# Kernel optimization log

Measured on AMD Instinct MI355X. Metric: run time of the kernel, lower is better.

Reference implementation:

```python
import jax, jax.numpy as jnp
import numpy as np

B, M, HID, NH = 2, 2048, 1024, 16
D = HID // NH  # 64


def setup_inputs() -> dict:
    key = jax.random.key(0)
    ks = jax.random.split(key, 6)
    s = 0.02  # weight init scale
    return {
        "h": jax.random.normal(ks[0], (B, M, HID), dtype=jnp.float32),
        "key_pe": jax.random.normal(ks[1], (1, D, M), dtype=jnp.float32) * s,
        "Wq": jax.random.normal(ks[2], (HID, HID), dtype=jnp.float32) * s,
        "Wk": jax.random.normal(ks[3], (HID, HID), dtype=jnp.float32) * s,
        "Wv": jax.random.normal(ks[4], (HID, HID), dtype=jnp.float32) * s,
        "Wo": jax.random.normal(ks[5], (HID, HID), dtype=jnp.float32) * s,
    }


def reference(h, key_pe, Wq, Wk, Wv, Wo):
    # Faithful to the source: in SelfAttention.forward the gathered-span scores
    # are overwritten by dense Q K^T, and the softmaxed `attn` is discarded;
    # the returned value is (Q K^T) V (no scaling, no softmax). key_pe only
    # feeds the dead softmax branch, so it does not affect the output.
    b, m, hd = h.shape
    nh, d = NH, hd // NH

    def heads(x):  # (B, M, HID) -> (B, NH, M, D)
        return x.reshape(b, m, nh, d).transpose(0, 2, 1, 3)

    q = heads(h @ Wq.T)
    k = heads(h @ Wk.T)
    v = heads(h @ Wv.T)

    attn_cont = jnp.einsum("bhqd,bhkd->bhqk", q, k)  # (B, NH, M, M)
    out = jnp.einsum("bhqk,bhkd->bhqd", attn_cont, v)  # (B, NH, M, D)
    out = out.transpose(0, 2, 1, 3).reshape(b, m, hd)  # (B, M, HID)
    return out @ Wo.T
```

## Files before the change

### kernel.cpp

```cpp
#include <hip/hip_runtime.h>
#include <hip/hip_bf16.h>


typedef unsigned short u16;
typedef unsigned int u32;
typedef __attribute__((ext_vector_type(8))) short bf16x8;
typedef __attribute__((ext_vector_type(4))) float f32x4;

__device__ __forceinline__ void async_copy16(void* lds, const void* g) {
  __builtin_amdgcn_global_load_lds((const __attribute__((address_space(1))) void*)g,
                                   (__attribute__((address_space(3))) void*)lds,
                                   16, 0, 0);
}

__device__ __forceinline__ u16 f2bf(float f) {
  union { __hip_bfloat16 h; u16 u; } c;
  c.h = __float2bfloat16(f);
  return c.u;
}
__device__ __forceinline__ float bflo(u32 w) {
  union { u32 u; float f; } c; c.u = w << 16; return c.f;
}
__device__ __forceinline__ float bfhi(u32 w) {
  union { u32 u; float f; } c; c.u = w & 0xFFFF0000u; return c.f;
}
__device__ __forceinline__ ushort4 cvt4(float4 v) {
  ushort4 o; o.x = f2bf(v.x); o.y = f2bf(v.y); o.z = f2bf(v.z); o.w = f2bf(v.w);
  return o;
}

template <int N> __device__ __forceinline__ void vw() {
  if constexpr (N == 8)      asm volatile("s_waitcnt vmcnt(8)" ::: "memory");
  else if constexpr (N == 4) asm volatile("s_waitcnt vmcnt(4)" ::: "memory");
  else if constexpr (N == 2) asm volatile("s_waitcnt vmcnt(2)" ::: "memory");
  else if constexpr (N == 0) asm volatile("s_waitcnt vmcnt(0)" ::: "memory");
}

__global__ __launch_bounds__(256) void prep(const float4* __restrict__ h,
                                            const float4* __restrict__ wq,
                                            const float4* __restrict__ wk,
                                            const float4* __restrict__ wv,
                                            ushort4* __restrict__ hb,
                                            ushort4* __restrict__ wcat) {
  int i = blockIdx.x * 256 + threadIdx.x;
  if (i < 1048576) { hb[i] = cvt4(h[i]); return; }
  i -= 1048576;
  if (i < 262144) { wcat[i] = cvt4(wq[i]); return; }
  i -= 262144;
  if (i < 262144) { wcat[262144 + i] = cvt4(wk[i]); return; }
  i -= 262144;
  wcat[524288 + i] = cvt4(wv[i]);
}


#define NOPW ((void)0)

#define PHASE(KT, DO_STAGE, VWAIT)                                           \
  do {                                                                       \
    const u16* Ab = &Als[(KT) & 3][wm * 32 + aoff];                          \
    const u16* Bb = &Bls[(KT) & 3][wn * 32 + aoff];                          \
    bf16x8 af[MI], bv[NI];                                                   \
    _Pragma("unroll") for (int i = 0; i < MI; ++i)                           \
        af[i] = *(const bf16x8*)(Ab + i * 512);                              \
    _Pragma("unroll") for (int j = 0; j < NI; ++j)                           \
        bv[j] = *(const bf16x8*)(Bb + j * 512);                              \
    DO_STAGE;                                                                \
    __builtin_amdgcn_s_setprio(1);                                           \
    _Pragma("unroll") for (int i = 0; i < MI; ++i)                           \
        _Pragma("unroll") for (int j = 0; j < NI; ++j)                       \
            acc[i][j] = __builtin_amdgcn_mfma_f32_16x16x32_bf16(             \
                af[i], bv[j], acc[i][j], 0, 0, 0);                           \
    __builtin_amdgcn_s_setprio(0);                                           \
    asm volatile("s_waitcnt lgkmcnt(0)" ::: "memory");                       \
    VWAIT;                                                                   \
    __builtin_amdgcn_s_barrier();                                            \
    __builtin_amdgcn_sched_barrier(0);                                       \
  } while (0)

template <bool BF16_OUT, int BN>
__global__ __launch_bounds__(512, 2) void gemm32(const u16* __restrict__ A,
                                                 int lda,
                                                 const u16* __restrict__ B0,
                                                 const u16* __restrict__ B1,
                                                 void* __restrict__ Cv,
                                                 int N) {
  constexpr int SA = 1;
  constexpr int SB = BN / 128;
  constexpr int V  = SA + SB;
  constexpr int MI = 4;
  constexpr int NI = BN / 4 / 16;

  __shared__ u16 Als[4][128 * 32];
  __shared__ u16 Bls[4][BN * 32];
  const int t = threadIdx.x;
  const int lane = t & 63;
  const int wave = t >> 6;
  const int wm = (wave >> 2) * 64;
  const int wn = (wave & 3) * (BN / 4);
  const int lrow = lane & 15;
  const int quad = lane >> 4;

  const int bid = blockIdx.x;
  const int m0 = (bid >> 3) * 128;
  const int n0 = (bid & 7) * BN;
  const u16* B = (B1 != nullptr && m0 >= 2048) ? B1 : B0;

  const int srow = lane >> 2;
  const int sgk  = (lane & 3) ^ ((lane >> 3) & 3);
  const u16* Ag = A + (size_t)(m0 + wave * (SA * 16) + srow) * lda + sgk * 8;
  const u16* Bg = B + (size_t)(n0 + wave * (SB * 16) + srow) * 1024 + sgk * 8;

  const int swz = (lrow >> 1) & 3;
  const int aoff = lrow * 32 + ((quad ^ swz) << 3);

  f32x4 acc[MI][NI];
#pragma unroll
  for (int i = 0; i < MI; ++i)
#pragma unroll
    for (int j = 0; j < NI; ++j) acc[i][j] = {0.f, 0.f, 0.f, 0.f};

  auto stage = [&](int kt) {
    const int buf = kt & 3;
#pragma unroll
    for (int j = 0; j < SA; ++j) {
      const int ch = wave * SA + j;
      async_copy16(&Als[buf][ch * 512 + lane * 8],
                   Ag + (size_t)(j * 16) * lda + kt * 32);
    }
#pragma unroll
    for (int j = 0; j < SB; ++j) {
      const int ch = wave * SB + j;
      async_copy16(&Bls[buf][ch * 512 + lane * 8],
                   Bg + (size_t)(j * 16) * 1024 + kt * 32);
    }
  };

  stage(0); stage(1); stage(2);
  vw<2 * V>();
  __builtin_amdgcn_s_barrier();
  __builtin_amdgcn_sched_barrier(0);

#pragma unroll 1
  for (int kt = 0; kt < 29; ++kt) {
    PHASE(kt, stage(kt + 3), vw<2 * V>());
  }
  PHASE(29, NOPW, vw<V>());
  PHASE(30, NOPW, vw<0>());
  PHASE(31, NOPW, NOPW);

  const int crow0 = m0 + wm + quad * 4;
  const int ccol0 = n0 + wn + lrow;
#pragma unroll
  for (int mf = 0; mf < MI; ++mf)
#pragma unroll
    for (int nf = 0; nf < NI; ++nf)
#pragma unroll
      for (int r = 0; r < 4; ++r) {
        const size_t idx = (size_t)(crow0 + mf * 16 + r) * N + ccol0 + nf * 16;
        if (BF16_OUT) ((u16*)Cv)[idx]   = f2bf(acc[mf][nf][r]);
        else          ((float*)Cv)[idx] = acc[mf][nf][r];
      }
}

__global__ __launch_bounds__(256) void s_kernel(const u16* __restrict__ QKV,
                                                float* __restrict__ Spart) {
  const int bh = blockIdx.x;
  const int b = bh >> 4, hh = bh & 15;
  const int row0 = b * 2048 + blockIdx.y * 128;
  const u16* Kg = QKV + (size_t)row0 * 3072 + 1024 + hh * 64;

  __shared__ float Ks[64][64];
  __shared__ float Vs[64][64];
  const int t = threadIdx.x;
  const int lr = t >> 2;
  const int lc = (t & 3) * 16;
  const int d1 = (t >> 4) * 4;
  const int d2 = (t & 15) * 4;

  float acc[4][4] = {};

  for (int r0 = 0; r0 < 128; r0 += 64) {
    const u16* kp = Kg + (size_t)(r0 + lr) * 3072 + lc;
    const uint4 kw0 = *(const uint4*)kp;
    const uint4 kw1 = *(const uint4*)(kp + 8);
    const uint4 vw0 = *(const uint4*)(kp + 1024);
    const uint4 vw1 = *(const uint4*)(kp + 1032);
    __syncthreads();
    float* kd = &Ks[lr][lc];
    *(float4*)(kd)      = float4{bflo(kw0.x), bfhi(kw0.x), bflo(kw0.y), bfhi(kw0.y)};
    *(float4*)(kd + 4)  = float4{bflo(kw0.z), bfhi(kw0.z), bflo(kw0.w), bfhi(kw0.w)};
    *(float4*)(kd + 8)  = float4{bflo(kw1.x), bfhi(kw1.x), bflo(kw1.y), bfhi(kw1.y)};
    *(float4*)(kd + 12) = float4{bflo(kw1.z), bfhi(kw1.z), bflo(kw1.w), bfhi(kw1.w)};
    float* vd = &Vs[lr][lc];
    *(float4*)(vd)      = float4{bflo(vw0.x), bfhi(vw0.x), bflo(vw0.y), bfhi(vw0.y)};
    *(float4*)(vd + 4)  = float4{bflo(vw0.z), bfhi(vw0.z), bflo(vw0.w), bfhi(vw0.w)};
    *(float4*)(vd + 8)  = float4{bflo(vw1.x), bfhi(vw1.x), bflo(vw1.y), bfhi(vw1.y)};
    *(float4*)(vd + 12) = float4{bflo(vw1.z), bfhi(vw1.z), bflo(vw1.w), bfhi(vw1.w)};
    __syncthreads();
#pragma unroll
    for (int r = 0; r < 64; ++r) {
      float kv[4], vv[4];
      *(float4*)kv = *(const float4*)&Ks[r][d1];
      *(float4*)vv = *(const float4*)&Vs[r][d2];
#pragma unroll
      for (int i = 0; i < 4; ++i)
#pragma unroll
        for (int j = 0; j < 4; ++j) acc[i][j] += kv[i] * vv[j];
    }
  }
  float* Sp = Spart + ((size_t)bh * 16 + blockIdx.y) * 4096;
#pragma unroll
  for (int i = 0; i < 4; ++i)
    *(float4*)&Sp[(d1 + i) * 64 + d2] =
        float4{acc[i][0], acc[i][1], acc[i][2], acc[i][3]};
}

__global__ __launch_bounds__(256) void reduce_s(const float4* __restrict__ Spart,
                                                float4* __restrict__ S) {
  const int g = blockIdx.x * 256 + threadIdx.x;
  const int bh = g >> 10, j = g & 1023;
  const float4* p = Spart + (size_t)bh * 16384 + j;
  float4 a = {0.f, 0.f, 0.f, 0.f};
#pragma unroll
  for (int c = 0; c < 16; ++c) {
    const float4 v = p[(size_t)c * 1024];
    a.x += v.x; a.y += v.y; a.z += v.z; a.w += v.w;
  }
  S[g] = a;
}

__global__ __launch_bounds__(256) void t_kernel(const float* __restrict__ S,
                                                const float* __restrict__ Wo,
                                                u16* __restrict__ Tt) {
  const int n0 = blockIdx.x * 128;
  const int hh = blockIdx.y;
  const int b  = blockIdx.z;
  __shared__ float Ss[64][68];
  __shared__ float Ws[128][68];
  const int t = threadIdx.x;
  {
    const float* sg = S + (size_t)(b * 16 + hh) * 4096 + (t >> 2) * 64 + (t & 3) * 16;
    float* sd = &Ss[t >> 2][(t & 3) * 16];
#pragma unroll
    for (int i = 0; i < 4; ++i) *(float4*)(sd + 4 * i) = *(const float4*)(sg + 4 * i);
    const float* wg = Wo + (size_t)(n0 + (t >> 1)) * 1024 + hh * 64 + (t & 1) * 32;
    float* wd = &Ws[t >> 1][(t & 1) * 32];
#pragma unroll
    for (int i = 0; i < 8; ++i) *(float4*)(wd + 4 * i) = *(const float4*)(wg + 4 * i);
  }
  __syncthreads();

  const int td = (t >> 4) * 4;
  const int tn = t & 15;
  float acc[4][8] = {};
  for (int jj = 0; jj < 64; jj += 4) {
    float4 sv[4], wv[8];
#pragma unroll
    for (int i = 0; i < 4; ++i) sv[i] = *(const float4*)&Ss[td + i][jj];
#pragma unroll
    for (int k = 0; k < 8; ++k) wv[k] = *(const float4*)&Ws[tn + 16 * k][jj];
#pragma unroll
    for (int i = 0; i < 4; ++i)
#pragma unroll
      for (int k = 0; k < 8; ++k)
        acc[i][k] += sv[i].x * wv[k].x + sv[i].y * wv[k].y +
                     sv[i].z * wv[k].z + sv[i].w * wv[k].w;
  }

  u16* tp = Tt + (size_t)b * 1048576;
#pragma unroll
  for (int k = 0; k < 8; ++k) {
    const int n = n0 + tn + 16 * k;
    ushort4 o;
    o.x = f2bf(acc[0][k]); o.y = f2bf(acc[1][k]);
    o.z = f2bf(acc[2][k]); o.w = f2bf(acc[3][k]);
    *(ushort4*)&tp[(size_t)n * 1024 + hh * 64 + td] = o;
  }
}

extern "C" void kernel_launch(void* const* d_in, const int* in_sizes, int n_in,
                              void* d_out, int out_size, void* d_ws, size_t ws_size,
                              hipStream_t stream) {
  const float* h  = (const float*)d_in[0];
  const float* Wq = (const float*)d_in[2];
  const float* Wk = (const float*)d_in[3];
  const float* Wv = (const float*)d_in[4];
  const float* Wo = (const float*)d_in[5];

  char* ws = (char*)d_ws;
  u16*   hb    = (u16*)(ws);
  u16*   wcat  = (u16*)(ws + (8ull  << 20));
  u16*   QKVb  = (u16*)(ws + (16ull << 20));
  float* S     = (float*)(ws + (40ull << 20));
  u16*   Tt    = (u16*)(ws + (41ull << 20));
  float* Spart = (float*)(ws + (48ull << 20));

  prep<<<7168, 256, 0, stream>>>((const float4*)h, (const float4*)Wq,
                                 (const float4*)Wk, (const float4*)Wv,
                                 (ushort4*)hb, (ushort4*)wcat);
  gemm32<true, 384><<<256, 512, 0, stream>>>(hb, 1024, wcat, nullptr,
                                             QKVb, 3072);
  s_kernel<<<dim3(32, 16), 256, 0, stream>>>(QKVb, Spart);
  reduce_s<<<128, 256, 0, stream>>>((const float4*)Spart, (float4*)S);
  t_kernel<<<dim3(8, 16, 2), 256, 0, stream>>>(S, Wo, Tt);
  gemm32<false, 128><<<256, 512, 0, stream>>>(QKVb, 3072, Tt, Tt + 1048576,
                                              d_out, 1024);
}
```

Baseline: 153.6 us.

## Retile GEMMs to 256-thread blocks with triple buffering and 512-block grids

Replaces the 512-thread, 4-stage GEMM with a new gemm32m template using 256-thread blocks, configurable BM/BN tiles, a 3-stage LDS ring and a prefetch distance of 2. The QKV projection now uses 128x192 tiles over 512 blocks with a swizzled n-tile mapping, and the output GEMM uses 64x128 tiles over 512 blocks. The aim is more blocks in flight per CU and less LDS per block, at the cost of shallower prefetch and less reuse per tile. It also leaves behind unused stubs (gemm_map, forward declarations of gemm1_k and gemm2_k, an altered gemm32).

```diff
diff --git a/kernel.cpp b/kernel.cpp
--- a/kernel.cpp
+++ b/kernel.cpp
@@ -30,8 +30,12 @@
 }
 
 template <int N> __device__ __forceinline__ void vw() {
-  if constexpr (N == 8)      asm volatile("s_waitcnt vmcnt(8)" ::: "memory");
+  if constexpr (N == 10)     asm volatile("s_waitcnt vmcnt(10)" ::: "memory");
+  else if constexpr (N == 8) asm volatile("s_waitcnt vmcnt(8)" ::: "memory");
+  else if constexpr (N == 6) asm volatile("s_waitcnt vmcnt(6)" ::: "memory");
+  else if constexpr (N == 5) asm volatile("s_waitcnt vmcnt(5)" ::: "memory");
   else if constexpr (N == 4) asm volatile("s_waitcnt vmcnt(4)" ::: "memory");
+  else if constexpr (N == 3) asm volatile("s_waitcnt vmcnt(3)" ::: "memory");
   else if constexpr (N == 2) asm volatile("s_waitcnt vmcnt(2)" ::: "memory");
   else if constexpr (N == 0) asm volatile("s_waitcnt vmcnt(0)" ::: "memory");
 }
@@ -57,8 +61,8 @@
 
 #define PHASE(KT, DO_STAGE, VWAIT)                                           \
   do {                                                                       \
-    const u16* Ab = &Als[(KT) & 3][wm * 32 + aoff];                          \
-    const u16* Bb = &Bls[(KT) & 3][wn * 32 + aoff];                          \
+    const u16* Ab = &Als[(KT) % 3][aoff];                                    \
+    const u16* Bb = &Bls[(KT) % 3][wn * 32 + aoff];                          \
     bf16x8 af[MI], bv[NI];                                                   \
     _Pragma("unroll") for (int i = 0; i < MI; ++i)                           \
         af[i] = *(const bf16x8*)(Ab + i * 512);                              \
@@ -77,38 +81,35 @@
     __builtin_amdgcn_sched_barrier(0);                                       \
   } while (0)
 
-template <bool BF16_OUT, int BN>
-__global__ __launch_bounds__(512, 2) void gemm32(const u16* __restrict__ A,
+template <bool BF16_OUT, int BM, int BN>
+__global__ __launch_bounds__(256, 2) void gemm32(const u16* __restrict__ A,
                                                  int lda,
                                                  const u16* __restrict__ B0,
                                                  const u16* __restrict__ B1,
                                                  void* __restrict__ Cv,
-                                                 int N) {
-  constexpr int SA = 1;
-  constexpr int SB = BN / 128;
+                                                 int N, int m0, int n0) {
+  static_assert(BM % 64 == 0 && BN % 64 == 0, "");
+  constexpr int SA = BM / 64;
+  constexpr int SB = BN / 64;
   constexpr int V  = SA + SB;
-  constexpr int MI = 4;
+  constexpr int MI = BM / 16;
   constexpr int NI = BN / 4 / 16;
 
-  __shared__ u16 Als[4][128 * 32];
-  __shared__ u16 Bls[4][BN * 32];
+  __shared__ u16 Als[3][BM * 32];
+  __shared__ u16 Bls[3][BN * 32];
   const int t = threadIdx.x;
   const int lane = t & 63;
   const int wave = t >> 6;
-  const int wm = (wave >> 2) * 64;
-  const int wn = (wave & 3) * (BN / 4);
+  const int wn = wave * (BN / 4);
   const int lrow = lane & 15;
   const int quad = lane >> 4;
 
-  const int bid = blockIdx.x;
-  const int m0 = (bid >> 3) * 128;
-  const int n0 = (bid & 7) * BN;
   const u16* B = (B1 != nullptr && m0 >= 2048) ? B1 : B0;
 
   const int srow = lane >> 2;
   const int sgk  = (lane & 3) ^ ((lane >> 3) & 3);
-  const u16* Ag = A + (size_t)(m0 + wave * (SA * 16) + srow) * lda + sgk * 8;
-  const u16* Bg = B + (size_t)(n0 + wave * (SB * 16) + srow) * 1024 + sgk * 8;
+  const u16* Ag = A + (size_t)(m0 + srow) * lda + sgk * 8;
+  const u16* Bg = B + (size_t)(n0 + srow) * 1024 + sgk * 8;
 
   const int swz = (lrow >> 1) & 3;
   const int aoff = lrow * 32 + ((quad ^ swz) << 3);
@@ -120,35 +121,152 @@
     for (int j = 0; j < NI; ++j) acc[i][j] = {0.f, 0.f, 0.f, 0.f};
 
   auto stage = [&](int kt) {
-    const int buf = kt & 3;
+    const int buf = kt % 3;
 #pragma unroll
     for (int j = 0; j < SA; ++j) {
-      const int ch = wave * SA + j;
+      const int ch = j * 4 + wave;
       async_copy16(&Als[buf][ch * 512 + lane * 8],
-                   Ag + (size_t)(j * 16) * lda + kt * 32);
+                   Ag + (size_t)(ch * 16) * lda + kt * 32);
     }
 #pragma unroll
     for (int j = 0; j < SB; ++j) {
-      const int ch = wave * SB + j;
+      const int ch = j * 4 + wave;
       async_copy16(&Bls[buf][ch * 512 + lane * 8],
-                   Bg + (size_t)(j * 16) * 1024 + kt * 32);
+                   Bg + (size_t)(ch * 16) * 1024 + kt * 32);
     }
   };
 
-  stage(0); stage(1); stage(2);
-  vw<2 * V>();
+  stage(0); stage(1);
+  vw<V>();
   __builtin_amdgcn_s_barrier();
   __builtin_amdgcn_sched_barrier(0);
 
 #pragma unroll 1
-  for (int kt = 0; kt < 29; ++kt) {
-    PHASE(kt, stage(kt + 3), vw<2 * V>());
-  }
-  PHASE(29, NOPW, vw<V>());
+  for (int kt = 0; kt < 30; ++kt) {
+    PHASE(kt, stage(kt + 2), vw<V>());
+  }
   PHASE(30, NOPW, vw<0>());
   PHASE(31, NOPW, NOPW);
 
-  const int crow0 = m0 + wm + quad * 4;
+  const int crow0 = m0 + quad * 4;
+  const int ccol0 = n0 + wn + lrow;
+#pragma unroll
+  for (int mf = 0; mf < MI; ++mf)
+#pragma unroll
+    for (int nf = 0; nf < NI; ++nf)
+#pragma unroll
+      for (int r = 0; r < 4; ++r) {
+        const size_t idx = (size_t)(crow0 + mf * 16 + r) * N + ccol0 + nf * 16;
+        if (BF16_OUT) ((u16*)Cv)[idx]   = f2bf(acc[mf][nf][r]);
+        else          ((float*)Cv)[idx] = acc[mf][nf][r];
+      }
+}
+
+__global__ __launch_bounds__(256, 2) void gemm1_k(const u16* __restrict__ A,
+                                                  const u16* __restrict__ B0,
+                                                  u16* __restrict__ C);
+__global__ __launch_bounds__(256, 2) void gemm2_k(const u16* __restrict__ A,
+                                                  const u16* __restrict__ B0,
+                                                  const u16* __restrict__ B1,
+                                                  float* __restrict__ C);
+
+template <bool BF16_OUT, int BM, int BN, int NT>
+__global__ __launch_bounds__(256, 2) void gemm_map(const u16* __restrict__ A,
+                                                   int lda,
+                                                   const u16* __restrict__ B0,
+                                                   const u16* __restrict__ B1,
+                                                   void* __restrict__ Cv,
+                                                   int N) {
+  const int bid = blockIdx.x;
+  int m0, n0;
+  if (NT == 16) {
+    m0 = (bid >> 4) * BM;
+    n0 = (((bid & 7) << 1) | ((bid >> 3) & 1)) * BN;
+  } else {
+    m0 = (bid >> 3) * BM;
+    n0 = (bid & 7) * BN;
+  }
+  extern __device__ void unreachable_();
+  (void)A; (void)lda; (void)B0; (void)B1; (void)Cv; (void)N; (void)m0; (void)n0;
+}
+
+template <bool BF16_OUT, int BM, int BN, int NT>
+__global__ __launch_bounds__(256, 2) void gemm32m(const u16* __restrict__ A,
+                                                  int lda,
+                                                  const u16* __restrict__ B0,
+                                                  const u16* __restrict__ B1,
+                                                  void* __restrict__ Cv,
+                                                  int N) {
+  static_assert(BM % 64 == 0 && BN % 64 == 0, "");
+  constexpr int SA = BM / 64;
+  constexpr int SB = BN / 64;
+  constexpr int V  = SA + SB;
+  constexpr int MI = BM / 16;
+  constexpr int NI = BN / 4 / 16;
+
+  __shared__ u16 Als[3][BM * 32];
+  __shared__ u16 Bls[3][BN * 32];
+  const int t = threadIdx.x;
+  const int lane = t & 63;
+  const int wave = t >> 6;
+  const int wn = wave * (BN / 4);
+  const int lrow = lane & 15;
+  const int quad = lane >> 4;
+
+  const int bid = blockIdx.x;
+  int m0, n0;
+  if constexpr (NT == 16) {
+    m0 = (bid >> 4) * BM;
+    n0 = ((((bid & 7) << 1) | ((bid >> 3) & 1))) * BN;
+  } else {
+    m0 = (bid >> 3) * BM;
+    n0 = (bid & 7) * BN;
+  }
+  const u16* B = (B1 != nullptr && m0 >= 2048) ? B1 : B0;
+
+  const int srow = lane >> 2;
+  const int sgk  = (lane & 3) ^ ((lane >> 3) & 3);
+  const u16* Ag = A + (size_t)(m0 + srow) * lda + sgk * 8;
+  const u16* Bg = B + (size_t)(n0 + srow) * 1024 + sgk * 8;
+
+  const int swz = (lrow >> 1) & 3;
+  const int aoff = lrow * 32 + ((quad ^ swz) << 3);
+
+  f32x4 acc[MI][NI];
+#pragma unroll
+  for (int i = 0; i < MI; ++i)
+#pragma unroll
+    for (int j = 0; j < NI; ++j) acc[i][j] = {0.f, 0.f, 0.f, 0.f};
+
+  auto stage = [&](int kt) {
+    const int buf = kt % 3;
+#pragma unroll
+    for (int j = 0; j < SA; ++j) {
+      const int ch = j * 4 + wave;
+      async_copy16(&Als[buf][ch * 512 + lane * 8],
+                   Ag + (size_t)(ch * 16) * lda + kt * 32);
+    }
+#pragma unroll
+    for (int j = 0; j < SB; ++j) {
+      const int ch = j * 4 + wave;
+      async_copy16(&Bls[buf][ch * 512 + lane * 8],
+                   Bg + (size_t)(ch * 16) * 1024 + kt * 32);
+    }
+  };
+
+  stage(0); stage(1);
+  vw<V>();
+  __builtin_amdgcn_s_barrier();
+  __builtin_amdgcn_sched_barrier(0);
+
+#pragma unroll 1
+  for (int kt = 0; kt < 30; ++kt) {
+    PHASE(kt, stage(kt + 2), vw<V>());
+  }
+  PHASE(30, NOPW, vw<0>());
+  PHASE(31, NOPW, NOPW);
+
+  const int crow0 = m0 + quad * 4;
   const int ccol0 = n0 + wn + lrow;
 #pragma unroll
   for (int mf = 0; mf < MI; ++mf)
@@ -298,11 +416,12 @@
   prep<<<7168, 256, 0, stream>>>((const float4*)h, (const float4*)Wq,
                                  (const float4*)Wk, (const float4*)Wv,
                                  (ushort4*)hb, (ushort4*)wcat);
-  gemm32<true, 384><<<256, 512, 0, stream>>>(hb, 1024, wcat, nullptr,
-                                             QKVb, 3072);
+  gemm32m<true, 128, 192, 16><<<512, 256, 0, stream>>>(hb, 1024, wcat,
+                                                       nullptr, QKVb, 3072);
   s_kernel<<<dim3(32, 16), 256, 0, stream>>>(QKVb, Spart);
   reduce_s<<<128, 256, 0, stream>>>((const float4*)Spart, (float4*)S);
   t_kernel<<<dim3(8, 16, 2), 256, 0, stream>>>(S, Wo, Tt);
-  gemm32<false, 128><<<256, 512, 0, stream>>>(QKVb, 3072, Tt, Tt + 1048576,
-                                              d_out, 1024);
-}
+  gemm32m<false, 64, 128, 8><<<512, 256, 0, stream>>>(QKVb, 3072, Tt,
+                                                      Tt + 1048576, d_out,
+                                                      1024);
+}
```

Measured after the change: 156.1 us. Within noise of the previous version (+1.6%).

## Fold Wq into per-batch K^T V matrices to drop the Q projection

Applied to the files above, without the earlier changes.

The Q projection is no longer computed. Per head, S^T = V^T K is folded with Wq to form R, then a new small GEMM forms X = Wo·R per batch, and the final GEMM multiplies bf16 h by X. The QKV GEMM shrinks to a KV GEMM with N=2048, and prep now converts Wo instead of Wq. This trades one large M×1024×1024 projection for a weight-sized 1024³ GEMM per batch, changing the rounding path in exchange for fewer FLOPs on the critical GEMMs.

```diff
diff --git a/kernel.cpp b/kernel.cpp
--- a/kernel.cpp
+++ b/kernel.cpp
@@ -31,25 +31,28 @@
 
 template <int N> __device__ __forceinline__ void vw() {
   if constexpr (N == 8)      asm volatile("s_waitcnt vmcnt(8)" ::: "memory");
+  else if constexpr (N == 6) asm volatile("s_waitcnt vmcnt(6)" ::: "memory");
   else if constexpr (N == 4) asm volatile("s_waitcnt vmcnt(4)" ::: "memory");
+  else if constexpr (N == 3) asm volatile("s_waitcnt vmcnt(3)" ::: "memory");
   else if constexpr (N == 2) asm volatile("s_waitcnt vmcnt(2)" ::: "memory");
   else if constexpr (N == 0) asm volatile("s_waitcnt vmcnt(0)" ::: "memory");
 }
 
 __global__ __launch_bounds__(256) void prep(const float4* __restrict__ h,
-                                            const float4* __restrict__ wq,
                                             const float4* __restrict__ wk,
                                             const float4* __restrict__ wv,
+                                            const float4* __restrict__ wo,
                                             ushort4* __restrict__ hb,
-                                            ushort4* __restrict__ wcat) {
+                                            ushort4* __restrict__ wcat,
+                                            ushort4* __restrict__ wob) {
   int i = blockIdx.x * 256 + threadIdx.x;
   if (i < 1048576) { hb[i] = cvt4(h[i]); return; }
   i -= 1048576;
-  if (i < 262144) { wcat[i] = cvt4(wq[i]); return; }
+  if (i < 262144) { wcat[i] = cvt4(wk[i]); return; }
   i -= 262144;
-  if (i < 262144) { wcat[262144 + i] = cvt4(wk[i]); return; }
+  if (i < 262144) { wcat[262144 + i] = cvt4(wv[i]); return; }
   i -= 262144;
-  wcat[524288 + i] = cvt4(wv[i]);
+  wob[i] = cvt4(wo[i]);
 }
 
 
@@ -78,12 +81,12 @@
   } while (0)
 
 template <bool BF16_OUT, int BN>
-__global__ __launch_bounds__(512, 2) void gemm32(const u16* __restrict__ A,
-                                                 int lda,
-                                                 const u16* __restrict__ B0,
-                                                 const u16* __restrict__ B1,
-                                                 void* __restrict__ Cv,
-                                                 int N) {
+__global__ __launch_bounds__(512, 2) void gemm512(const u16* __restrict__ A,
+                                                  int lda,
+                                                  const u16* __restrict__ B0,
+                                                  const u16* __restrict__ B1,
+                                                  void* __restrict__ Cv,
+                                                  int N) {
   constexpr int SA = 1;
   constexpr int SB = BN / 128;
   constexpr int V  = SA + SB;
@@ -162,12 +165,129 @@
       }
 }
 
-__global__ __launch_bounds__(256) void s_kernel(const u16* __restrict__ QKV,
+__global__ __launch_bounds__(256, 2) void gemmX(const u16* __restrict__ A,
+                                                const u16* __restrict__ B0,
+                                                u16* __restrict__ C0) {
+  constexpr int SA = 1, SB = 2, V = 3;
+  constexpr int MI = 4, NI = 2;
+
+  __shared__ u16 Als[3][64 * 32];
+  __shared__ u16 Bls[3][128 * 32];
+  const int t = threadIdx.x;
+  const int lane = t & 63;
+  const int wave = t >> 6;
+  const int wn = wave * 32;
+  const int lrow = lane & 15;
+  const int quad = lane >> 4;
+
+  const int bid = blockIdx.x;
+  const int b  = bid >> 7;
+  const int m0 = ((bid >> 3) & 15) * 64;
+  const int n0 = (bid & 7) * 128;
+  const u16* B = B0 + (size_t)b * 1048576;
+  u16* C = C0 + (size_t)b * 1048576;
+
+  const int srow = lane >> 2;
+  const int sgk  = (lane & 3) ^ ((lane >> 3) & 3);
+  const u16* Ag = A + (size_t)(m0 + srow) * 1024 + sgk * 8;
+  const u16* Bg = B + (size_t)(n0 + srow) * 1024 + sgk * 8;
+
+  const int swz = (lrow >> 1) & 3;
+  const int aoff = lrow * 32 + ((quad ^ swz) << 3);
+
+  f32x4 acc[MI][NI];
+#pragma unroll
+  for (int i = 0; i < MI; ++i)
+#pragma unroll
+    for (int j = 0; j < NI; ++j) acc[i][j] = {0.f, 0.f, 0.f, 0.f};
+
+  auto stage = [&](int kt) {
+    const int buf = kt % 3;
+#pragma unroll
+    for (int j = 0; j < SA; ++j) {
+      const int ch = j * 4 + wave;
+      async_copy16(&Als[buf][ch * 512 + lane * 8],
+                   Ag + (size_t)(ch * 16) * 1024 + kt * 32);
+    }
+#pragma unroll
+    for (int j = 0; j < SB; ++j) {
+      const int ch = j * 4 + wave;
+      async_copy16(&Bls[buf][ch * 512 + lane * 8],
+                   Bg + (size_t)(ch * 16) * 1024 + kt * 32);
+    }
+  };
+
+  stage(0); stage(1);
+  vw<V>();
+  __builtin_amdgcn_s_barrier();
+  __builtin_amdgcn_sched_barrier(0);
+
+#pragma unroll 1
+  for (int kt = 0; kt < 30; ++kt) {
+    const int wm = 0; (void)wm;
+    do {
+      const u16* Ab = &Als[kt % 3][aoff];
+      const u16* Bb = &Bls[kt % 3][wn * 32 + aoff];
+      bf16x8 af[MI], bv[NI];
+#pragma unroll
+      for (int i = 0; i < MI; ++i) af[i] = *(const bf16x8*)(Ab + i * 512);
+#pragma unroll
+      for (int j = 0; j < NI; ++j) bv[j] = *(const bf16x8*)(Bb + j * 512);
+      stage(kt + 2);
+      __builtin_amdgcn_s_setprio(1);
+#pragma unroll
+      for (int i = 0; i < MI; ++i)
+#pragma unroll
+        for (int j = 0; j < NI; ++j)
+          acc[i][j] = __builtin_amdgcn_mfma_f32_16x16x32_bf16(
+              af[i], bv[j], acc[i][j], 0, 0, 0);
+      __builtin_amdgcn_s_setprio(0);
+      asm volatile("s_waitcnt lgkmcnt(0)" ::: "memory");
+      vw<V>();
+      __builtin_amdgcn_s_barrier();
+      __builtin_amdgcn_sched_barrier(0);
+    } while (0);
+  }
+  for (int kt = 30; kt < 32; ++kt) {
+    const u16* Ab = &Als[kt % 3][aoff];
+    const u16* Bb = &Bls[kt % 3][wn * 32 + aoff];
+    bf16x8 af[MI], bv[NI];
+#pragma unroll
+    for (int i = 0; i < MI; ++i) af[i] = *(const bf16x8*)(Ab + i * 512);
+#pragma unroll
+    for (int j = 0; j < NI; ++j) bv[j] = *(const bf16x8*)(Bb + j * 512);
+    __builtin_amdgcn_s_setprio(1);
+#pragma unroll
+    for (int i = 0; i < MI; ++i)
+#pragma unroll
+      for (int j = 0; j < NI; ++j)
+        acc[i][j] = __builtin_amdgcn_mfma_f32_16x16x32_bf16(
+            af[i], bv[j], acc[i][j], 0, 0, 0);
+    __builtin_amdgcn_s_setprio(0);
+    asm volatile("s_waitcnt lgkmcnt(0)" ::: "memory");
+    if (kt == 30) vw<0>();
+    __builtin_amdgcn_s_barrier();
+    __builtin_amdgcn_sched_barrier(0);
+  }
+
+  const int crow0 = m0 + quad * 4;
+  const int ccol0 = n0 + wn + lrow;
+#pragma unroll
+  for (int mf = 0; mf < MI; ++mf)
+#pragma unroll
+    for (int nf = 0; nf < NI; ++nf)
+#pragma unroll
+      for (int r = 0; r < 4; ++r)
+        C[(size_t)(crow0 + mf * 16 + r) * 1024 + ccol0 + nf * 16] =
+            f2bf(acc[mf][nf][r]);
+}
+
+__global__ __launch_bounds__(256) void s_kernel(const u16* __restrict__ KV,
                                                 float* __restrict__ Spart) {
   const int bh = blockIdx.x;
   const int b = bh >> 4, hh = bh & 15;
   const int row0 = b * 2048 + blockIdx.y * 128;
-  const u16* Kg = QKV + (size_t)row0 * 3072 + 1024 + hh * 64;
+  const u16* Kg = KV + (size_t)row0 * 2048 + hh * 64;
 
   __shared__ float Ks[64][64];
   __shared__ float Vs[64][64];
@@ -180,7 +300,7 @@
   float acc[4][4] = {};
 
   for (int r0 = 0; r0 < 128; r0 += 64) {
-    const u16* kp = Kg + (size_t)(r0 + lr) * 3072 + lc;
+    const u16* kp = Kg + (size_t)(r0 + lr) * 2048 + lc;
     const uint4 kw0 = *(const uint4*)kp;
     const uint4 kw1 = *(const uint4*)(kp + 8);
     const uint4 vw0 = *(const uint4*)(kp + 1024);
@@ -216,65 +336,78 @@
 }
 
 __global__ __launch_bounds__(256) void reduce_s(const float4* __restrict__ Spart,
-                                                float4* __restrict__ S) {
+                                                float* __restrict__ St) {
   const int g = blockIdx.x * 256 + threadIdx.x;
-  const int bh = g >> 10, j = g & 1023;
-  const float4* p = Spart + (size_t)bh * 16384 + j;
+  const int bh = g >> 10, j4 = g & 1023;
+  const float4* p = Spart + (size_t)bh * 16384 + j4;
   float4 a = {0.f, 0.f, 0.f, 0.f};
 #pragma unroll
   for (int c = 0; c < 16; ++c) {
     const float4 v = p[(size_t)c * 1024];
     a.x += v.x; a.y += v.y; a.z += v.z; a.w += v.w;
   }
-  S[g] = a;
-}
-
-__global__ __launch_bounds__(256) void t_kernel(const float* __restrict__ S,
-                                                const float* __restrict__ Wo,
-                                                u16* __restrict__ Tt) {
-  const int n0 = blockIdx.x * 128;
+  const int d = j4 >> 4;
+  const int j0 = (4 * j4) & 63;
+  float* o = St + (size_t)bh * 4096 + d;
+  o[(size_t)(j0 + 0) * 64] = a.x;
+  o[(size_t)(j0 + 1) * 64] = a.y;
+  o[(size_t)(j0 + 2) * 64] = a.z;
+  o[(size_t)(j0 + 3) * 64] = a.w;
+}
+
+__global__ __launch_bounds__(256) void r_kernel(const float* __restrict__ St,
+                                                const float* __restrict__ Wq,
+                                                u16* __restrict__ R) {
+  const int k0 = blockIdx.x * 128;
   const int hh = blockIdx.y;
   const int b  = blockIdx.z;
   __shared__ float Ss[64][68];
   __shared__ float Ws[128][68];
   const int t = threadIdx.x;
   {
-    const float* sg = S + (size_t)(b * 16 + hh) * 4096 + (t >> 2) * 64 + (t & 3) * 16;
+    const float* sg = St + (size_t)(b * 16 + hh) * 4096 + (t >> 2) * 64 + (t & 3) * 16;
     float* sd = &Ss[t >> 2][(t & 3) * 16];
 #pragma unroll
     for (int i = 0; i < 4; ++i) *(float4*)(sd + 4 * i) = *(const float4*)(sg + 4 * i);
-    const float* wg = Wo + (size_t)(n0 + (t >> 1)) * 1024 + hh * 64 + (t & 1) * 32;
-    float* wd = &Ws[t >> 1][(t & 1) * 32];
-#pragma unroll
-    for (int i = 0; i < 8; ++i) *(float4*)(wd + 4 * i) = *(const float4*)(wg + 4 * i);
+    const int d = t >> 2;
+    const int cs = (t & 3) * 32;
+    const float* wg = Wq + (size_t)(hh * 64 + d) * 1024 + k0 + cs;
+#pragma unroll
+    for (int i = 0; i < 8; ++i) {
+      const float4 v = *(const float4*)(wg + 4 * i);
+      Ws[cs + 4 * i + 0][d] = v.x;
+      Ws[cs + 4 * i + 1][d] = v.y;
+      Ws[cs + 4 * i + 2][d] = v.z;
+      Ws[cs + 4 * i + 3][d] = v.w;
+    }
   }
   __syncthreads();
 
-  const int td = (t >> 4) * 4;
-  const int tn = t & 15;
+  const int tj = (t >> 4) * 4;
+  const int tk = t & 15;
   float acc[4][8] = {};
-  for (int jj = 0; jj < 64; jj += 4) {
+  for (int dd = 0; dd < 64; dd += 4) {
     float4 sv[4], wv[8];
 #pragma unroll
-    for (int i = 0; i < 4; ++i) sv[i] = *(const float4*)&Ss[td + i][jj];
-#pragma unroll
-    for (int k = 0; k < 8; ++k) wv[k] = *(const float4*)&Ws[tn + 16 * k][jj];
+    for (int i = 0; i < 4; ++i) sv[i] = *(const float4*)&Ss[tj + i][dd];
+#pragma unroll
+    for (int q = 0; q < 8; ++q) wv[q] = *(const float4*)&Ws[tk + 16 * q][dd];
 #pragma unroll
     for (int i = 0; i < 4; ++i)
 #pragma unroll
-      for (int k = 0; k < 8; ++k)
-        acc[i][k] += sv[i].x * wv[k].x + sv[i].y * wv[k].y +
-                     sv[i].z * wv[k].z + sv[i].w * wv[k].w;
-  }
-
-  u16* tp = Tt + (size_t)b * 1048576;
-#pragma unroll
-  for (int k = 0; k < 8; ++k) {
-    const int n = n0 + tn + 16 * k;
+      for (int q = 0; q < 8; ++q)
+        acc[i][q] += sv[i].x * wv[q].x + sv[i].y * wv[q].y +
+                     sv[i].z * wv[q].z + sv[i].w * wv[q].w;
+  }
+
+  u16* rp = R + (size_t)b * 1048576;
+#pragma unroll
+  for (int q = 0; q < 8; ++q) {
+    const int k = k0 + tk + 16 * q;
     ushort4 o;
-    o.x = f2bf(acc[0][k]); o.y = f2bf(acc[1][k]);
-    o.z = f2bf(acc[2][k]); o.w = f2bf(acc[3][k]);
-    *(ushort4*)&tp[(size_t)n * 1024 + hh * 64 + td] = o;
+    o.x = f2bf(acc[0][q]); o.y = f2bf(acc[1][q]);
+    o.z = f2bf(acc[2][q]); o.w = f2bf(acc[3][q]);
+    *(ushort4*)&rp[(size_t)k * 1024 + hh * 64 + tj] = o;
   }
 }
 
@@ -290,19 +423,22 @@
   char* ws = (char*)d_ws;
   u16*   hb    = (u16*)(ws);
   u16*   wcat  = (u16*)(ws + (8ull  << 20));
-  u16*   QKVb  = (u16*)(ws + (16ull << 20));
-  float* S     = (float*)(ws + (40ull << 20));
-  u16*   Tt    = (u16*)(ws + (41ull << 20));
-  float* Spart = (float*)(ws + (48ull << 20));
-
-  prep<<<7168, 256, 0, stream>>>((const float4*)h, (const float4*)Wq,
-                                 (const float4*)Wk, (const float4*)Wv,
-                                 (ushort4*)hb, (ushort4*)wcat);
-  gemm32<true, 384><<<256, 512, 0, stream>>>(hb, 1024, wcat, nullptr,
-                                             QKVb, 3072);
-  s_kernel<<<dim3(32, 16), 256, 0, stream>>>(QKVb, Spart);
-  reduce_s<<<128, 256, 0, stream>>>((const float4*)Spart, (float4*)S);
-  t_kernel<<<dim3(8, 16, 2), 256, 0, stream>>>(S, Wo, Tt);
-  gemm32<false, 128><<<256, 512, 0, stream>>>(QKVb, 3072, Tt, Tt + 1048576,
-                                              d_out, 1024);
-}
+  u16*   wob   = (u16*)(ws + (12ull << 20));
+  u16*   KVb   = (u16*)(ws + (16ull << 20));
+  float* St    = (float*)(ws + (40ull << 20));
+  u16*   R     = (u16*)(ws + (41ull << 20));
+  u16*   X     = (u16*)(ws + (45ull << 20));
+  float* Spart = (float*)(ws + (56ull << 20));
+
+  prep<<<7168, 256, 0, stream>>>((const float4*)h, (const float4*)Wk,
+                                 (const float4*)Wv, (const float4*)Wo,
+                                 (ushort4*)hb, (ushort4*)wcat, (ushort4*)wob);
+  gemm512<true, 256><<<256, 512, 0, stream>>>(hb, 1024, wcat, nullptr,
+                                              KVb, 2048);
+  s_kernel<<<dim3(32, 16), 256, 0, stream>>>(KVb, Spart);
+  reduce_s<<<128, 256, 0, stream>>>((const float4*)Spart, St);
+  r_kernel<<<dim3(8, 16, 2), 256, 0, stream>>>(St, Wq, R);
+  gemmX<<<256, 256, 0, stream>>>(wob, R, X);
+  gemm512<false, 128><<<256, 512, 0, stream>>>(hb, 1024, X, X + 1048576,
+                                               d_out, 1024);
+}
```

Result: slower. 159.4 us (+3.8%).
